# Kernel optimization log

Hardware: AMD Instinct MI355X
Metric: run time of the kernel (lower is better)

## Reference

```python
import jax, jax.numpy as jnp
import numpy as np

N_NODES = 100000
N_EDGES = 500000
HIDDEN = 256


def setup_inputs() -> dict:
    key = jax.random.key(0)
    k_x, k_e, k_w1, k_b1, k_w2, k_b2 = jax.random.split(key, 6)
    x = jax.random.normal(k_x, (N_NODES, HIDDEN), dtype=jnp.float32)
    edge_label_index = jax.random.randint(k_e, (2, N_EDGES), 0, N_NODES, dtype=jnp.int64)
    # fc1: Linear(2*hidden -> hidden); fc2: Linear(hidden -> 1). PyTorch stores W as [out, in].
    bound1 = 1.0 / np.sqrt(2 * HIDDEN)
    W1 = jax.random.uniform(k_w1, (HIDDEN, 2 * HIDDEN), dtype=jnp.float32, minval=-bound1, maxval=bound1)
    b1 = jax.random.uniform(k_b1, (HIDDEN,), dtype=jnp.float32, minval=-bound1, maxval=bound1)
    bound2 = 1.0 / np.sqrt(HIDDEN)
    W2 = jax.random.uniform(k_w2, (1, HIDDEN), dtype=jnp.float32, minval=-bound2, maxval=bound2)
    b2 = jax.random.uniform(k_b2, (1,), dtype=jnp.float32, minval=-bound2, maxval=bound2)
    return {"x": x, "edge_label_index": edge_label_index, "W1": W1, "b1": b1, "W2": W2, "b2": b2}


def reference(x, edge_label_index, W1, b1, W2, b2):
    # Gather endpoint features: [E, H] each
    feat_src = x[edge_label_index[0]]
    feat_dst = x[edge_label_index[1]]
    h = jnp.concatenate([feat_src, feat_dst], axis=1)  # [E, 2H]
    h = jax.nn.relu(h @ W1.T + b1)                      # [E, H]
    out = jax.nn.sigmoid(h @ W2.T + b2)                 # [E, 1]
    return out.reshape(-1)
```

## Files before the change

kernel.cpp:

```cpp
#include <hip/hip_runtime.h>
#include <math.h>

#define NNODES 100000
#define MT     64
#define NTILES 1563
#define NODESP (NTILES * MT)
#define NEDGES 500000
#define HID    256
#define K2     512
#define GEMM_GRID 256
#define MT2    32
#define NT2    3125

typedef _Float16 h8v __attribute__((ext_vector_type(8)));
typedef _Float16 h2v __attribute__((ext_vector_type(2)));
typedef __bf16   bf16x8 __attribute__((ext_vector_type(8)));
typedef float    f32x4  __attribute__((ext_vector_type(4)));

__device__ __forceinline__ unsigned short f2bf(float f) {
    unsigned int u = __float_as_uint(f);
    u += 0x7FFFu + ((u >> 16) & 1u);
    return (unsigned short)(u >> 16);
}

__device__ __forceinline__ void gload16(const float* g, const float* lds_base_uniform) {
    typedef const __attribute__((address_space(1))) unsigned int ga_u32;
    typedef __attribute__((address_space(3))) unsigned int lds_u32;
    __builtin_amdgcn_global_load_lds((ga_u32*)(uintptr_t)g,
                                     (lds_u32*)(unsigned int)(uintptr_t)lds_base_uniform,
                                     16, 0, 0);
}

__global__ void cvt_w1h(const float* __restrict__ W1, _Float16* __restrict__ Bsw) {
    int t = blockIdx.x * 256 + threadIdx.x;
    if (t >= 8 * 32 * 64) return;
    int lane = t & 63, nt = (t >> 6) & 31, kt = t >> 11;
    int j = nt * 16 + (lane & 15);
    int k = kt * 32 + ((lane >> 4) << 3);
    const float* src = W1 + (size_t)(j & 255) * K2 + ((j >> 8) << 8) + k;
    union { _Float16 s[8]; uint4 v; } u;
#pragma unroll
    for (int jj = 0; jj < 8; ++jj) u.s[jj] = (_Float16)src[jj];
    ((uint4*)Bsw)[t] = u.v;
}

__global__ void cvt_w2p(const float* __restrict__ W2, float* __restrict__ w2p) {
    int t = threadIdx.x;
    int i = (t >> 2) & 15, nt = t & 3;
    w2p[t] = W2[(t & ~63) | (nt * 16 + i)];
}

__global__ __launch_bounds__(512, 1) void node_gemm8(
    const float* __restrict__ x,
    const _Float16* __restrict__ Bsw,
    const float* __restrict__ b1,
    _Float16* __restrict__ UV)
{
    __shared__ __align__(16) float A0[MT2 * 256];
    __shared__ __align__(16) float A1[MT2 * 256];
    const int tid  = threadIdx.x;
    const int lane = tid & 63;
    const int wave = tid >> 6;

    const h8v* B8 = (const h8v*)Bsw;
    h8v barr[8][4];
#pragma unroll
    for (int ks = 0; ks < 8; ++ks)
#pragma unroll
        for (int nt = 0; nt < 4; ++nt)
            barr[ks][nt] = B8[((size_t)(ks * 32 + wave * 4 + nt)) * 64 + lane];

    float b1v[4];
#pragma unroll
    for (int nt = 0; nt < 4; ++nt) {
        int col = wave * 64 + nt * 16 + (lane & 15);
        b1v[nt] = (col < 256) ? b1[col] : 0.0f;
    }

    auto stage = [&](int t, float* dstb) {
#pragma unroll
        for (int i = 0; i < 4; ++i) {
            int row = wave * 4 + i;
            int u   = lane ^ (row & 7);
            const float* src = x + (size_t)(t * MT2 + row) * 256 + u * 4;
            gload16(src, dstb + row * 256);
        }
    };

    auto work = [&](const float* Ab, int t) {
        const f32x4* A4 = (const f32x4*)Ab;
        f32x4 acc[2][4] = {};
#pragma unroll
        for (int ks = 0; ks < 8; ++ks) {
            h8v af[2];
#pragma unroll
            for (int mt = 0; mt < 2; ++mt) {
                int row = mt * 16 + (lane & 15);
                int u0  = ks * 8 + ((lane >> 4) << 1);
                f32x4 lo = A4[row * 64 + ( u0      ^ (row & 7))];
                f32x4 hi = A4[row * 64 + ((u0 + 1) ^ (row & 7))];
                af[mt] = h8v{(_Float16)lo[0], (_Float16)lo[1], (_Float16)lo[2], (_Float16)lo[3],
                             (_Float16)hi[0], (_Float16)hi[1], (_Float16)hi[2], (_Float16)hi[3]};
            }
#pragma unroll
            for (int mt = 0; mt < 2; ++mt)
#pragma unroll
                for (int nt = 0; nt < 4; ++nt)
                    acc[mt][nt] = __builtin_amdgcn_mfma_f32_16x16x32_f16(
                        af[mt], barr[ks][nt], acc[mt][nt], 0, 0, 0);
        }
#pragma unroll
        for (int mt = 0; mt < 2; ++mt) {
#pragma unroll
            for (int r = 0; r < 4; ++r) {
                int row = t * MT2 + mt * 16 + ((lane >> 4) << 2) + r;
                union { _Float16 h[4]; uint2 v; } pk;
#pragma unroll
                for (int nt = 0; nt < 4; ++nt)
                    pk.h[nt] = (_Float16)(acc[mt][nt][r] + b1v[nt]);
                *(uint2*)(UV + (size_t)row * 512 + wave * 64 + (lane & 15) * 4) = pk.v;
            }
        }
    };

    int tile = blockIdx.x;
    stage(tile, A0);
    __syncthreads();

    for (;;) {
        int n1 = tile + GEMM_GRID;
        if (n1 < NT2) stage(n1, A1);
        work(A0, tile);
        if (n1 >= NT2) return;
        __syncthreads();

        int n2 = n1 + GEMM_GRID;
        if (n2 < NT2) stage(n2, A0);
        work(A1, n1);
        if (n2 >= NT2) return;
        __syncthreads();
        tile = n2;
    }
}

__global__ __launch_bounds__(256) void edge_out4(
    const _Float16* __restrict__ UV,
    const int* __restrict__ ei,
    const float* __restrict__ w2p,
    const float* __restrict__ b2,
    float* __restrict__ out)
{
    const int tid = threadIdx.x;
    const int q   = tid & 31;
    const int g   = tid >> 5;
    const long e  = (long)blockIdx.x * 32 + g * 4;

    int4 s4 = *(const int4*)(ei + e);
    int4 d4 = *(const int4*)(ei + NEDGES + e);

    h2v w2h[4];
    {
        const float4* pw = (const float4*)w2p + q * 2;
        float4 c = pw[0], d = pw[1];
        w2h[0] = h2v{(_Float16)c.x, (_Float16)c.y};
        w2h[1] = h2v{(_Float16)c.z, (_Float16)c.w};
        w2h[2] = h2v{(_Float16)d.x, (_Float16)d.y};
        w2h[3] = h2v{(_Float16)d.z, (_Float16)d.w};
    }

    union U8 { uint4 v; h2v h[4]; };
    const _Float16* up = UV + q * 8;

    U8 uu[4], vv[4];
    uu[0].v = *(const uint4*)(up + (size_t)s4.x * 512);
    vv[0].v = *(const uint4*)(up + (size_t)d4.x * 512 + 256);
    uu[1].v = *(const uint4*)(up + (size_t)s4.y * 512);
    vv[1].v = *(const uint4*)(up + (size_t)d4.y * 512 + 256);
    uu[2].v = *(const uint4*)(up + (size_t)s4.z * 512);
    vv[2].v = *(const uint4*)(up + (size_t)d4.z * 512 + 256);
    uu[3].v = *(const uint4*)(up + (size_t)s4.w * 512);
    vv[3].v = *(const uint4*)(up + (size_t)d4.w * 512 + 256);

    const h2v zz = {(_Float16)0.0f, (_Float16)0.0f};
    float z[4] = {0.f, 0.f, 0.f, 0.f};
#pragma unroll
    for (int ed = 0; ed < 4; ++ed) {
#pragma unroll
        for (int p = 0; p < 4; ++p) {
            h2v h = uu[ed].h[p] + vv[ed].h[p];
            h = __builtin_elementwise_max(h, zz);
            z[ed] = __builtin_amdgcn_fdot2(h, w2h[p], z[ed], false);
        }
    }
#pragma unroll
    for (int m = 1; m < 32; m <<= 1) {
        z[0] += __shfl_xor(z[0], m, 32);
        z[1] += __shfl_xor(z[1], m, 32);
        z[2] += __shfl_xor(z[2], m, 32);
        z[3] += __shfl_xor(z[3], m, 32);
    }
    if (q < 4) {
        float zq = (q == 0) ? z[0] : (q == 1) ? z[1] : (q == 2) ? z[2] : z[3];
        out[e + q] = 1.0f / (1.0f + expf(-(zq + b2[0])));
    }
}

__global__ void cvt_w1_r1(const float* __restrict__ W1, unsigned short* __restrict__ Bsw) {
    int t = blockIdx.x * 256 + threadIdx.x;
    if (t >= 16 * 16 * 64) return;
    int lane = t & 63, nt = (t >> 6) & 15, kt = t >> 10;
    int n = nt * 16 + (lane & 15);
    int k = kt * 32 + ((lane >> 4) << 3);
    const float* src = W1 + (size_t)n * K2 + k;
    union { unsigned short s[8]; uint4 v; } u;
#pragma unroll
    for (int j = 0; j < 8; ++j) u.s[j] = f2bf(src[j]);
    ((uint4*)Bsw)[t] = u.v;
}

__global__ __launch_bounds__(256) void edge_mlp_fb(
    const float* __restrict__ xf, const int* __restrict__ ei,
    const unsigned short* __restrict__ Bsw, const float* __restrict__ b1,
    const float* __restrict__ W2, const float* __restrict__ b2,
    float* __restrict__ out)
{
    __shared__ __align__(16) unsigned short Asw[8 * 4 * 64 * 8];
    __shared__ float es[64];
    const int tid = threadIdx.x, lane = tid & 63, wave = tid >> 6;
    const int e0 = blockIdx.x * 64;
    if (tid < 64) es[tid] = 0.0f;
    f32x4 acc[4][4] = {};
    const bf16x8* A8 = (const bf16x8*)Asw;
    const bf16x8* B8 = (const bf16x8*)Bsw;
    for (int h = 0; h < 2; ++h) {
#pragma unroll
        for (int i = 0; i < 8; ++i) {
            int m = i * 8 + wave * 2 + (lane >> 5);
            int e = e0 + m;
            int ee = (e < NEDGES) ? e : 0;
            int node = ei[(size_t)h * NEDGES + ee];
            int chunk = lane & 31;
            const float4* p = (const float4*)(xf + ((size_t)node << 8) + (chunk << 3));
            float4 a = p[0], bq = p[1];
            union { unsigned short s[8]; uint4 v4; } u;
            u.s[0] = f2bf(a.x);  u.s[1] = f2bf(a.y);  u.s[2] = f2bf(a.z);  u.s[3] = f2bf(a.w);
            u.s[4] = f2bf(bq.x); u.s[5] = f2bf(bq.y); u.s[6] = f2bf(bq.z); u.s[7] = f2bf(bq.w);
            int ktl = chunk >> 2, qq = chunk & 3;
            int u16 = ((ktl * 4 + (m >> 4)) << 6) + (qq << 4) + (m & 15);
            u16 ^= (u16 >> 8) & 7;
            ((uint4*)Asw)[u16] = u.v4;
        }
        __syncthreads();
#pragma unroll
        for (int kt = 0; kt < 8; ++kt) {
            bf16x8 af[4], bfr[4];
#pragma unroll
            for (int mt = 0; mt < 4; ++mt) {
                int u16 = ((kt * 4 + mt) << 6) + lane;
                u16 ^= (u16 >> 8) & 7;
                af[mt] = A8[u16];
            }
#pragma unroll
            for (int nt = 0; nt < 4; ++nt)
                bfr[nt] = B8[(((h * 8 + kt) << 4) + (wave << 2) + nt) * 64 + lane];
#pragma unroll
            for (int mt = 0; mt < 4; ++mt)
#pragma unroll
                for (int nt = 0; nt < 4; ++nt)
                    acc[mt][nt] = __builtin_amdgcn_mfma_f32_16x16x32_bf16(
                        af[mt], bfr[nt], acc[mt][nt], 0, 0, 0);
        }
        __syncthreads();
    }
    float w2v[4], b1v[4];
#pragma unroll
    for (int nt = 0; nt < 4; ++nt) {
        int n = (wave << 6) + (nt << 4) + (lane & 15);
        w2v[nt] = W2[n]; b1v[nt] = b1[n];
    }
#pragma unroll
    for (int mt = 0; mt < 4; ++mt) {
#pragma unroll
        for (int r = 0; r < 4; ++r) {
            float p = 0.0f;
#pragma unroll
            for (int nt = 0; nt < 4; ++nt) {
                float hv = acc[mt][nt][r] + b1v[nt];
                p = fmaf(fmaxf(hv, 0.0f), w2v[nt], p);
            }
            p += __shfl_xor(p, 1, 16);
            p += __shfl_xor(p, 2, 16);
            p += __shfl_xor(p, 4, 16);
            p += __shfl_xor(p, 8, 16);
            if ((lane & 15) == 0)
                atomicAdd(&es[(mt << 4) + ((lane >> 4) << 2) + r], p);
        }
    }
    __syncthreads();
    if (tid < 64) {
        int e = e0 + tid;
        if (e < NEDGES) out[e] = 1.0f / (1.0f + expf(-(es[tid] + b2[0])));
    }
}

extern "C" void kernel_launch(void* const* d_in, const int* in_sizes, int n_in,
                              void* d_out, int out_size, void* d_ws, size_t ws_size,
                              hipStream_t stream) {
    const float* x  = (const float*)d_in[0];
    const int*   ei = (const int*)d_in[1];
    const float* W1 = (const float*)d_in[2];
    const float* b1 = (const float*)d_in[3];
    const float* W2 = (const float*)d_in[4];
    const float* b2 = (const float*)d_in[5];
    float* out = (float*)d_out;

    const size_t BSW_BYTES = 1 << 18;
    const size_t W2P_BYTES = 4096;
    const size_t UV_BYTES  = (size_t)NODESP * K2 * 2;
    const size_t NEED_A = BSW_BYTES + W2P_BYTES + UV_BYTES;

    if (ws_size >= NEED_A) {
        _Float16* Bsw = (_Float16*)d_ws;
        float*    w2p = (float*)((char*)d_ws + BSW_BYTES);
        _Float16* UV  = (_Float16*)((char*)d_ws + BSW_BYTES + W2P_BYTES);
        cvt_w1h<<<64, 256, 0, stream>>>(W1, Bsw);
        cvt_w2p<<<1, 256, 0, stream>>>(W2, w2p);
        node_gemm8<<<GEMM_GRID, 512, 0, stream>>>(x, Bsw, b1, UV);
        edge_out4<<<NEDGES / 32, 256, 0, stream>>>(UV, ei, w2p, b2, out);
    } else {
        unsigned short* Bsw = (unsigned short*)d_ws;
        cvt_w1_r1<<<64, 256, 0, stream>>>(W1, Bsw);
        edge_mlp_fb<<<(NEDGES + 63) / 64, 256, 0, stream>>>(x, ei, Bsw, b1, W2, b2, out);
    }
}
```

Before: 243.7 us.

## Fold weight conversion kernels into GEMM and edge kernels, process 8 edges per group

Removes the two small weight-conversion launches by having the node GEMM read and convert W1 from fp32 directly into registers, and having the edge kernel gather and permute W2 itself. The edge kernel now handles 8 edges per 32-lane group instead of 4, which halves the grid and puts more gathers in flight per thread. The last block clamps its edge offset, so a few edges get recomputed and written twice. Each GEMM block now reads fp32 W1 with strided loads instead of a pre-swizzled fp16 buffer, and the edge kernel uses more registers.

Result: slower. 258.7 us (+6.2%).

```diff
diff --git a/kernel.cpp b/kernel.cpp
--- a/kernel.cpp
+++ b/kernel.cpp
@@ -31,28 +31,9 @@
                                      16, 0, 0);
 }
 
-__global__ void cvt_w1h(const float* __restrict__ W1, _Float16* __restrict__ Bsw) {
-    int t = blockIdx.x * 256 + threadIdx.x;
-    if (t >= 8 * 32 * 64) return;
-    int lane = t & 63, nt = (t >> 6) & 31, kt = t >> 11;
-    int j = nt * 16 + (lane & 15);
-    int k = kt * 32 + ((lane >> 4) << 3);
-    const float* src = W1 + (size_t)(j & 255) * K2 + ((j >> 8) << 8) + k;
-    union { _Float16 s[8]; uint4 v; } u;
-#pragma unroll
-    for (int jj = 0; jj < 8; ++jj) u.s[jj] = (_Float16)src[jj];
-    ((uint4*)Bsw)[t] = u.v;
-}
-
-__global__ void cvt_w2p(const float* __restrict__ W2, float* __restrict__ w2p) {
-    int t = threadIdx.x;
-    int i = (t >> 2) & 15, nt = t & 3;
-    w2p[t] = W2[(t & ~63) | (nt * 16 + i)];
-}
-
-__global__ __launch_bounds__(512, 1) void node_gemm8(
+__global__ __launch_bounds__(512, 1) void node_gemm9(
     const float* __restrict__ x,
-    const _Float16* __restrict__ Bsw,
+    const float* __restrict__ W1,
     const float* __restrict__ b1,
     _Float16* __restrict__ UV)
 {
@@ -62,13 +43,19 @@
     const int lane = tid & 63;
     const int wave = tid >> 6;
 
-    const h8v* B8 = (const h8v*)Bsw;
     h8v barr[8][4];
 #pragma unroll
     for (int ks = 0; ks < 8; ++ks)
 #pragma unroll
-        for (int nt = 0; nt < 4; ++nt)
-            barr[ks][nt] = B8[((size_t)(ks * 32 + wave * 4 + nt)) * 64 + lane];
+        for (int nt = 0; nt < 4; ++nt) {
+            int j = (wave * 4 + nt) * 16 + (lane & 15);
+            const float* src = W1 + (size_t)(j & 255) * K2 + ((j >> 8) << 8)
+                             + ks * 32 + ((lane >> 4) << 3);
+            float4 a = ((const float4*)src)[0];
+            float4 b = ((const float4*)src)[1];
+            barr[ks][nt] = h8v{(_Float16)a.x, (_Float16)a.y, (_Float16)a.z, (_Float16)a.w,
+                               (_Float16)b.x, (_Float16)b.y, (_Float16)b.z, (_Float16)b.w};
+        }
 
     float b1v[4];
 #pragma unroll
@@ -143,48 +130,56 @@
     }
 }
 
-__global__ __launch_bounds__(256) void edge_out4(
+__global__ __launch_bounds__(256) void edge_out5(
     const _Float16* __restrict__ UV,
     const int* __restrict__ ei,
-    const float* __restrict__ w2p,
+    const float* __restrict__ W2,
     const float* __restrict__ b2,
     float* __restrict__ out)
 {
     const int tid = threadIdx.x;
     const int q   = tid & 31;
     const int g   = tid >> 5;
-    const long e  = (long)blockIdx.x * 32 + g * 4;
-
-    int4 s4 = *(const int4*)(ei + e);
-    int4 d4 = *(const int4*)(ei + NEDGES + e);
+    long e = (long)blockIdx.x * 64 + g * 8;
+    if (e > NEDGES - 8) e = NEDGES - 8;
+
+    int4 sa = *(const int4*)(ei + e);
+    int4 sb = *(const int4*)(ei + e + 4);
+    int4 da = *(const int4*)(ei + NEDGES + e);
+    int4 db = *(const int4*)(ei + NEDGES + e + 4);
 
     h2v w2h[4];
     {
-        const float4* pw = (const float4*)w2p + q * 2;
-        float4 c = pw[0], d = pw[1];
-        w2h[0] = h2v{(_Float16)c.x, (_Float16)c.y};
-        w2h[1] = h2v{(_Float16)c.z, (_Float16)c.w};
-        w2h[2] = h2v{(_Float16)d.x, (_Float16)d.y};
-        w2h[3] = h2v{(_Float16)d.z, (_Float16)d.w};
+        float w2f[8];
+#pragma unroll
+        for (int jj = 0; jj < 8; ++jj) {
+            int t   = q * 8 + jj;
+            int col = (t & ~63) | (((t & 3) << 4) | ((t >> 2) & 15));
+            w2f[jj] = W2[col];
+        }
+        w2h[0] = h2v{(_Float16)w2f[0], (_Float16)w2f[1]};
+        w2h[1] = h2v{(_Float16)w2f[2], (_Float16)w2f[3]};
+        w2h[2] = h2v{(_Float16)w2f[4], (_Float16)w2f[5]};
+        w2h[3] = h2v{(_Float16)w2f[6], (_Float16)w2f[7]};
     }
 
     union U8 { uint4 v; h2v h[4]; };
     const _Float16* up = UV + q * 8;
 
-    U8 uu[4], vv[4];
-    uu[0].v = *(const uint4*)(up + (size_t)s4.x * 512);
-    vv[0].v = *(const uint4*)(up + (size_t)d4.x * 512 + 256);
-    uu[1].v = *(const uint4*)(up + (size_t)s4.y * 512);
-    vv[1].v = *(const uint4*)(up + (size_t)d4.y * 512 + 256);
-    uu[2].v = *(const uint4*)(up + (size_t)s4.z * 512);
-    vv[2].v = *(const uint4*)(up + (size_t)d4.z * 512 + 256);
-    uu[3].v = *(const uint4*)(up + (size_t)s4.w * 512);
-    vv[3].v = *(const uint4*)(up + (size_t)d4.w * 512 + 256);
+    int s[8] = {sa.x, sa.y, sa.z, sa.w, sb.x, sb.y, sb.z, sb.w};
+    int d[8] = {da.x, da.y, da.z, da.w, db.x, db.y, db.z, db.w};
+
+    U8 uu[8], vv[8];
+#pragma unroll
+    for (int ed = 0; ed < 8; ++ed) {
+        uu[ed].v = *(const uint4*)(up + (size_t)s[ed] * 512);
+        vv[ed].v = *(const uint4*)(up + (size_t)d[ed] * 512 + 256);
+    }
 
     const h2v zz = {(_Float16)0.0f, (_Float16)0.0f};
-    float z[4] = {0.f, 0.f, 0.f, 0.f};
-#pragma unroll
-    for (int ed = 0; ed < 4; ++ed) {
+    float z[8] = {};
+#pragma unroll
+    for (int ed = 0; ed < 8; ++ed) {
 #pragma unroll
         for (int p = 0; p < 4; ++p) {
             h2v h = uu[ed].h[p] + vv[ed].h[p];
@@ -194,13 +189,15 @@
     }
 #pragma unroll
     for (int m = 1; m < 32; m <<= 1) {
-        z[0] += __shfl_xor(z[0], m, 32);
-        z[1] += __shfl_xor(z[1], m, 32);
-        z[2] += __shfl_xor(z[2], m, 32);
-        z[3] += __shfl_xor(z[3], m, 32);
-    }
-    if (q < 4) {
-        float zq = (q == 0) ? z[0] : (q == 1) ? z[1] : (q == 2) ? z[2] : z[3];
+#pragma unroll
+        for (int ed = 0; ed < 8; ++ed)
+            z[ed] += __shfl_xor(z[ed], m, 32);
+    }
+    if (q < 8) {
+        float zq = z[0];
+#pragma unroll
+        for (int ed = 1; ed < 8; ++ed)
+            if (q == ed) zq = z[ed];
         out[e + q] = 1.0f / (1.0f + expf(-(zq + b2[0])));
     }
 }
@@ -314,19 +311,12 @@
     const float* b2 = (const float*)d_in[5];
     float* out = (float*)d_out;
 
-    const size_t BSW_BYTES = 1 << 18;
-    const size_t W2P_BYTES = 4096;
-    const size_t UV_BYTES  = (size_t)NODESP * K2 * 2;
-    const size_t NEED_A = BSW_BYTES + W2P_BYTES + UV_BYTES;
-
-    if (ws_size >= NEED_A) {
-        _Float16* Bsw = (_Float16*)d_ws;
-        float*    w2p = (float*)((char*)d_ws + BSW_BYTES);
-        _Float16* UV  = (_Float16*)((char*)d_ws + BSW_BYTES + W2P_BYTES);
-        cvt_w1h<<<64, 256, 0, stream>>>(W1, Bsw);
-        cvt_w2p<<<1, 256, 0, stream>>>(W2, w2p);
-        node_gemm8<<<GEMM_GRID, 512, 0, stream>>>(x, Bsw, b1, UV);
-        edge_out4<<<NEDGES / 32, 256, 0, stream>>>(UV, ei, w2p, b2, out);
+    const size_t UV_BYTES = (size_t)NODESP * K2 * 2;
+
+    if (ws_size >= UV_BYTES) {
+        _Float16* UV = (_Float16*)d_ws;
+        node_gemm9<<<GEMM_GRID, 512, 0, stream>>>(x, W1, b1, UV);
+        edge_out5<<<(NEDGES + 63) / 64, 256, 0, stream>>>(UV, ei, W2, b2, out);
     } else {
         unsigned short* Bsw = (unsigned short*)d_ws;
         cvt_w1_r1<<<64, 256, 0, stream>>>(W1, Bsw);
```
